# Kernel optimization log

Hardware: AMD Instinct MI355X
Metric: run time of the kernel (lower is better)

Reference implementation:

```python
import jax, jax.numpy as jnp
import numpy as np

EPS = 1e-5

def _ln(x, g, b):
    m = jnp.mean(x, axis=-1, keepdims=True)
    v = jnp.var(x, axis=-1, keepdims=True)
    return (x - m) * jax.lax.rsqrt(v + EPS) * g + b

def _lrelu(x):
    return jnp.where(x >= 0, x, 0.2 * x)

def _xavier(k, shape):
    a = (6.0 / (shape[0] + shape[1])) ** 0.5
    return jax.random.uniform(k, shape, minval=-a, maxval=a, dtype=jnp.float32)

def setup_inputs() -> dict:
    key = jax.random.key(0)
    ks = jax.random.split(key, 10)
    B, P, I = 32, 2048, 4096          # batch, n_pathway, n_img_features
    HQ, QK, HV, L = 64, 64, 64, 256   # hidden_dim_q(==qk), hidden_dim_qk, hidden_dim_v, classifier latent
    return {
        "img": jax.random.normal(ks[0], (B, 4, I), jnp.float32),
        "pathway": jax.random.normal(ks[1], (B, P), jnp.float32),
        "qw": _xavier(ks[2], (1, HQ)),
        "qw2": _xavier(ks[3], (HQ, QK)),
        "kw": _xavier(ks[4], (4, QK)),
        "vw": _xavier(ks[5], (4, HV)),
        "vw2": jax.random.normal(ks[6], (HV, 1), jnp.float32) * (HV ** -0.5),
        "q_g": jnp.ones(QK, jnp.float32), "q_b": jnp.zeros(QK, jnp.float32),
        "k_g": jnp.ones(QK, jnp.float32), "k_b": jnp.zeros(QK, jnp.float32),
        "v_g": jnp.ones(HV, jnp.float32), "v_b": jnp.zeros(HV, jnp.float32),
        "n1_g": jnp.ones(P, jnp.float32), "n1_b": jnp.zeros(P, jnp.float32),
        "n2_g": jnp.ones(L, jnp.float32), "n2_b": jnp.zeros(L, jnp.float32),
        "w1": _xavier(ks[7], (L, P)), "b1": jnp.zeros(L, jnp.float32),
        "w2": jax.random.normal(ks[8], (1, L), jnp.float32) * (L ** -0.5),
        "b2": jnp.zeros(1, jnp.float32),
    }

def reference(img, pathway, qw, qw2, kw, vw, vw2,
              q_g, q_b, k_g, k_b, v_g, v_b, n1_g, n1_b, n2_g, n2_b,
              w1, b1, w2, b2):
    P = pathway.shape[1]
    vrf = (P ** 0.5) / 2.0            # gamma * sqrt(n_pathway) / 2, gamma=1.0
    C = 0.5                           # soft_sign_constant
    img_t = jnp.swapaxes(img, -2, -1)              # [B, I, 4]
    # query path: outer product with [1, HQ] weight, LN, leaky, second proj, leaky (source applies key_relu to query)
    qm = pathway[..., None] @ qw                   # [B, P, HQ]
    qm = _lrelu(_ln(qm, q_g, q_b))
    qm = _lrelu(qm @ qw2)                          # [B, P, QK]
    # key path: LN only (source never relu's the key matrix)
    km = _ln(img_t @ kw, k_g, k_b)                 # [B, I, QK]
    # value path
    vm = _lrelu(_ln(img_t @ vw, v_g, v_b)) @ vw2   # [B, I, 1]
    # relu + variance-scale + soft-sign attention
    attn = jnp.einsum('bpd,bid->bpi', qm, km)      # [B, P, I]
    attn = jax.nn.relu(attn) / vrf
    attn = attn / (jnp.abs(attn) + C)
    out = attn @ vm                                # [B, P, 1]
    # classifier head (dropout = identity in eval)
    h = _lrelu(_ln(out[..., 0], n1_g, n1_b))       # [B, P]
    h = _lrelu(_ln(h @ w1.T + b1, n2_g, n2_b))     # [B, L]
    logits = h @ w2.T + b2                         # [B, 1]
    return (logits, attn, out)
```

## Files before the change

### kernel.cpp

```cpp
#include <hip/hip_runtime.h>
#include <hip/hip_bf16.h>

#define EPS 1e-5f
#define INV_VRF 4.4194173824159220e-02f

#define NB 32
#define NP 2048
#define NI 4096
#define ND 64
#define NL 256

#define ATTN_OFF 32L
#define OUT_OFF  268435488L

typedef __attribute__((ext_vector_type(4))) float vf4;
typedef __attribute__((ext_vector_type(4))) short vs4;
typedef __attribute__((ext_vector_type(8))) short vs8;

__device__ __forceinline__ unsigned short f2bf(float f) {
  unsigned int u = __float_as_uint(f);
  unsigned int r = (u + 0x7FFFu + ((u >> 16) & 1u)) >> 16;
  return (unsigned short)r;
}

__device__ __forceinline__ void gload16(const void* g, void* l) {
  __builtin_amdgcn_global_load_lds(
      (const __attribute__((address_space(1))) unsigned int*)g,
      (__attribute__((address_space(3))) unsigned int*)l, 16, 0, 0);
}

__global__ __launch_bounds__(256) void k_qm(
    const float* __restrict__ pathway, const float* __restrict__ qw,
    const float* __restrict__ qw2, const float* __restrict__ q_g,
    const float* __restrict__ q_b, unsigned short* __restrict__ qm)
{
  __shared__ float qw2s[64 * 64];
  int tid = threadIdx.x, lane = tid & 63, w = tid >> 6;
  for (int idx = tid; idx < 4096; idx += 256) qw2s[idx] = qw2[idx];
  float qwv = qw[lane], qg = q_g[lane], qb = q_b[lane];
  float s1 = qwv, s2 = qwv * qwv;
  #pragma unroll
  for (int m = 32; m; m >>= 1) { s1 += __shfl_xor(s1, m); s2 += __shfl_xor(s2, m); }
  float mq = s1 * (1.f / 64.f), vq = s2 * (1.f / 64.f) - mq * mq;
  float qc = qwv - mq;
  __syncthreads();
  long base = (long)blockIdx.x * 32 + w * 8;
  for (int r = 0; r < 8; ++r) {
    long row = base + r;
    float s = pathway[row];
    float alpha = s * rsqrtf(s * s * vq + EPS);
    float t = alpha * qc * qg + qb;
    t = t >= 0.f ? t : 0.2f * t;
    float acc = 0.f;
    #pragma unroll
    for (int h = 0; h < 64; ++h) acc += __shfl(t, h) * qw2s[h * 64 + lane];
    acc = acc >= 0.f ? acc : 0.2f * acc;
    qm[row * 64 + lane] = f2bf(acc);
  }
}

__global__ __launch_bounds__(256) void k_kmvm(
    const float* __restrict__ img, const float* __restrict__ kw,
    const float* __restrict__ vw, const float* __restrict__ vw2,
    const float* __restrict__ k_g, const float* __restrict__ k_b,
    const float* __restrict__ v_g, const float* __restrict__ v_b,
    unsigned short* __restrict__ km, float* __restrict__ vm)
{
  int tid = threadIdx.x, lane = tid & 63, w = tid >> 6;
  long row = (long)blockIdx.x * 4 + w;
  int b = (int)(row >> 12), i = (int)(row & 4095);
  const float* ib = img + (long)b * 4 * 4096 + i;
  float xv = (lane < 4) ? ib[lane * 4096] : 0.f;
  float x0 = __shfl(xv, 0), x1 = __shfl(xv, 1), x2 = __shfl(xv, 2), x3 = __shfl(xv, 3);
  int d = lane;
  float kp = x0 * kw[d] + x1 * kw[64 + d] + x2 * kw[128 + d] + x3 * kw[192 + d];
  float vp = x0 * vw[d] + x1 * vw[64 + d] + x2 * vw[128 + d] + x3 * vw[192 + d];
  float a1 = kp, a2 = kp * kp, a3 = vp, a4 = vp * vp;
  #pragma unroll
  for (int m = 32; m; m >>= 1) {
    a1 += __shfl_xor(a1, m); a2 += __shfl_xor(a2, m);
    a3 += __shfl_xor(a3, m); a4 += __shfl_xor(a4, m);
  }
  float mk = a1 * (1.f / 64.f), vk = a2 * (1.f / 64.f) - mk * mk;
  float mv = a3 * (1.f / 64.f), vv = a4 * (1.f / 64.f) - mv * mv;
  float kmv = (kp - mk) * rsqrtf(vk + EPS) * k_g[d] + k_b[d];
  km[row * 64 + d] = f2bf(kmv);
  float y = (vp - mv) * rsqrtf(vv + EPS) * v_g[d] + v_b[d];
  y = y >= 0.f ? y : 0.2f * y;
  float pv = y * vw2[d];
  #pragma unroll
  for (int m = 32; m; m >>= 1) pv += __shfl_xor(pv, m);
  if (lane == 0) vm[row] = pv;
}

__global__ __launch_bounds__(256) void k_attn(
    const unsigned short* __restrict__ qm, const unsigned short* __restrict__ km,
    const float* __restrict__ vm, float* __restrict__ dout)
{
  __shared__ __align__(16) unsigned short qm_s[64 * 64];
  __shared__ __align__(16) unsigned short km_s[2][64 * 64];
  int tid = threadIdx.x, lane = tid & 63, w = tid >> 6;
  int g = lane >> 4, c = lane & 15;
  int bid = blockIdx.x, b = bid >> 5, pt = bid & 31;
  long p_base = (long)b * NP + pt * 64;
  const char* qsrc = (const char*)(qm + p_base * 64);
  const char* ksrc = (const char*)(km + (long)b * NI * 64);

  #pragma unroll
  for (int j = 0; j < 2; ++j) {
    int o = w * 2048 + j * 1024 + (lane << 4);
    gload16(qsrc + o, (char*)qm_s + w * 2048 + j * 1024);
  }
  #pragma unroll
  for (int j = 0; j < 2; ++j) {
    int o = w * 2048 + j * 1024 + (lane << 4);
    int so = o ^ ((((o >> 7) & 7)) << 4);
    gload16(ksrc + so, (char*)km_s[0] + w * 2048 + j * 1024);
  }
  __syncthreads();

  vs8 afr[2];
  {
    const char* qrow = (const char*)qm_s + (w * 16 + c) * 128;
    #pragma unroll
    for (int kk = 0; kk < 2; ++kk) {
      vs4 lo = *(const vs4*)(qrow + kk * 64 + 8 * g);
      vs4 hi = *(const vs4*)(qrow + kk * 64 + 32 + 8 * g);
      vs8 a;
      a[0] = lo[0]; a[1] = lo[1]; a[2] = lo[2]; a[3] = lo[3];
      a[4] = hi[0]; a[5] = hi[1]; a[6] = hi[2]; a[7] = hi[3];
      afr[kk] = a;
    }
  }
  float* rp[4];
  #pragma unroll
  for (int r = 0; r < 4; ++r)
    rp[r] = dout + ATTN_OFF + (p_base + w * 16 + g * 4 + r) * (long)NI;
  const float* vmb = vm + (long)b * NI;
  float oacc[4] = {0.f, 0.f, 0.f, 0.f};
  int swz = (c & 7) << 4;

  for (int s = 0; s < 64; ++s) {
    int cur = s & 1;
    if (s < 63) {
      #pragma unroll
      for (int j = 0; j < 2; ++j) {
        int o = w * 2048 + j * 1024 + (lane << 4);
        int so = o ^ ((((o >> 7) & 7)) << 4);
        gload16(ksrc + (s + 1) * 8192 + so,
                (char*)km_s[cur ^ 1] + w * 2048 + j * 1024);
      }
    }
    vf4 acc[4];
    #pragma unroll
    for (int nt = 0; nt < 4; ++nt) acc[nt] = (vf4){0.f, 0.f, 0.f, 0.f};
    #pragma unroll
    for (int kk = 0; kk < 2; ++kk) {
      #pragma unroll
      for (int nt = 0; nt < 4; ++nt) {
        const char* krow = (const char*)km_s[cur] + (nt * 16 + c) * 128;
        vs4 lo = *(const vs4*)(krow + ((kk * 64 + 8 * g) ^ swz));
        vs4 hi = *(const vs4*)(krow + ((kk * 64 + 32 + 8 * g) ^ swz));
        vs8 bf;
        bf[0] = lo[0]; bf[1] = lo[1]; bf[2] = lo[2]; bf[3] = lo[3];
        bf[4] = hi[0]; bf[5] = hi[1]; bf[6] = hi[2]; bf[7] = hi[3];
        acc[nt] = __builtin_amdgcn_mfma_f32_16x16x32_bf16(afr[kk], bf, acc[nt], 0, 0, 0);
      }
    }
    int ib0 = s * 64;
    float vmv[4];
    #pragma unroll
    for (int nt = 0; nt < 4; ++nt) vmv[nt] = vmb[ib0 + nt * 16 + c];
    #pragma unroll
    for (int r = 0; r < 4; ++r) {
      float* rpr = rp[r];
      #pragma unroll
      for (int nt = 0; nt < 4; ++nt) {
        int col = ib0 + nt * 16 + c;
        float x = acc[nt][r];
        x = fmaxf(x, 0.f) * INV_VRF;
        float y = x * __builtin_amdgcn_rcpf(x + 0.5f);
        rpr[col] = y;
        oacc[r] += y * vmv[nt];
      }
    }
    __syncthreads();
  }
  #pragma unroll
  for (int m = 1; m <= 8; m <<= 1) {
    #pragma unroll
    for (int r = 0; r < 4; ++r) oacc[r] += __shfl_xor(oacc[r], m);
  }
  if (c == 0) {
    #pragma unroll
    for (int r = 0; r < 4; ++r)
      dout[OUT_OFF + p_base + w * 16 + g * 4 + r] = oacc[r];
  }
}

__global__ __launch_bounds__(256) void k_head(
    const float* __restrict__ n1_g, const float* __restrict__ n1_b,
    const float* __restrict__ n2_g, const float* __restrict__ n2_b,
    const float* __restrict__ w1, const float* __restrict__ b1,
    const float* __restrict__ w2, const float* __restrict__ b2,
    float* __restrict__ dout)
{
  int tid = threadIdx.x, lane = tid & 63, w = tid >> 6;
  int b = blockIdx.x;
  __shared__ float h1s[2048];
  __shared__ float red[8];
  const float* orow = dout + OUT_OFF + (long)b * NP;
  float vals[8];
  float s1 = 0.f, s2 = 0.f;
  #pragma unroll
  for (int j = 0; j < 8; ++j) {
    float v = orow[j * 256 + tid];
    vals[j] = v; s1 += v; s2 += v * v;
  }
  #pragma unroll
  for (int m = 32; m; m >>= 1) { s1 += __shfl_xor(s1, m); s2 += __shfl_xor(s2, m); }
  if (lane == 0) { red[w] = s1; red[4 + w] = s2; }
  __syncthreads();
  float S1 = red[0] + red[1] + red[2] + red[3];
  float S2 = red[4] + red[5] + red[6] + red[7];
  float mean = S1 * (1.f / 2048.f);
  float var = S2 * (1.f / 2048.f) - mean * mean;
  float rs = rsqrtf(var + EPS);
  __syncthreads();
  #pragma unroll
  for (int j = 0; j < 8; ++j) {
    int p = j * 256 + tid;
    float h = (vals[j] - mean) * rs * n1_g[p] + n1_b[p];
    h = h >= 0.f ? h : 0.2f * h;
    h1s[p] = h;
  }
  __syncthreads();
  float acc = b1[tid];
  const float* wr = w1 + (long)tid * 2048;
  for (int q = 0; q < 2048; q += 4) {
    float4 wv = *(const float4*)(wr + q);
    acc += wv.x * h1s[q] + wv.y * h1s[q + 1] + wv.z * h1s[q + 2] + wv.w * h1s[q + 3];
  }
  float t1 = acc, t2 = acc * acc;
  #pragma unroll
  for (int m = 32; m; m >>= 1) { t1 += __shfl_xor(t1, m); t2 += __shfl_xor(t2, m); }
  if (lane == 0) { red[w] = t1; red[4 + w] = t2; }
  __syncthreads();
  float T1 = red[0] + red[1] + red[2] + red[3];
  float T2 = red[4] + red[5] + red[6] + red[7];
  float m2 = T1 * (1.f / 256.f);
  float v2 = T2 * (1.f / 256.f) - m2 * m2;
  float rs2 = rsqrtf(v2 + EPS);
  float h2 = (acc - m2) * rs2 * n2_g[tid] + n2_b[tid];
  h2 = h2 >= 0.f ? h2 : 0.2f * h2;
  float lg = h2 * w2[tid];
  #pragma unroll
  for (int m = 32; m; m >>= 1) lg += __shfl_xor(lg, m);
  __syncthreads();
  if (lane == 0) red[w] = lg;
  __syncthreads();
  if (tid == 0) dout[b] = red[0] + red[1] + red[2] + red[3] + b2[0];
}

extern "C" void kernel_launch(void* const* d_in, const int* in_sizes, int n_in,
                              void* d_out, int out_size, void* d_ws, size_t ws_size,
                              hipStream_t stream)
{
  const float* img     = (const float*)d_in[0];
  const float* pathway = (const float*)d_in[1];
  const float* qw      = (const float*)d_in[2];
  const float* qw2     = (const float*)d_in[3];
  const float* kw      = (const float*)d_in[4];
  const float* vw      = (const float*)d_in[5];
  const float* vw2     = (const float*)d_in[6];
  const float* q_g     = (const float*)d_in[7];
  const float* q_b     = (const float*)d_in[8];
  const float* k_g     = (const float*)d_in[9];
  const float* k_b     = (const float*)d_in[10];
  const float* v_g     = (const float*)d_in[11];
  const float* v_b     = (const float*)d_in[12];
  const float* n1_g    = (const float*)d_in[13];
  const float* n1_b    = (const float*)d_in[14];
  const float* n2_g    = (const float*)d_in[15];
  const float* n2_b    = (const float*)d_in[16];
  const float* w1      = (const float*)d_in[17];
  const float* b1      = (const float*)d_in[18];
  const float* w2      = (const float*)d_in[19];
  const float* b2      = (const float*)d_in[20];
  float* dout = (float*)d_out;

  unsigned short* qm_ws = (unsigned short*)d_ws;
  unsigned short* km_ws = (unsigned short*)((char*)d_ws + 8388608);
  float*          vm_ws = (float*)((char*)d_ws + 25165824);

  k_qm<<<dim3(2048), dim3(256), 0, stream>>>(pathway, qw, qw2, q_g, q_b, qm_ws);
  k_kmvm<<<dim3(32768), dim3(256), 0, stream>>>(img, kw, vw, vw2, k_g, k_b, v_g, v_b, km_ws, vm_ws);
  k_attn<<<dim3(1024), dim3(256), 0, stream>>>(qm_ws, km_ws, vm_ws, dout);
  k_head<<<dim3(32), dim3(256), 0, stream>>>(n1_g, n1_b, n2_g, n2_b, w1, b1, w2, b2, dout);
}
```

Measured before the change: 500.3 us.

## Transpose attn tile through LDS for vectorized nontemporal stores, remap blocks

The attention kernel now stages each MFMA output tile through a per-wave swizzled LDS buffer, so every lane writes 16-byte contiguous chunks of attn with nontemporal stores instead of scattered 4-byte stores. The vm loads become float4, and the out reduction shrinks to two shuffles. The block index is remapped (bid&7)*128 + bid>>3, likely to spread batches across XCDs for better L2 locality of km. The __syncthreads are replaced by explicit waitcnt/s_barrier, and the partial vmcnt(8) wait is meant to let stores stay in flight across iterations. These manual waitcnt counts carry a correctness risk if the instruction ordering changes.

```diff
diff --git a/kernel.cpp b/kernel.cpp
--- a/kernel.cpp
+++ b/kernel.cpp
@@ -99,9 +99,12 @@
 {
   __shared__ __align__(16) unsigned short qm_s[64 * 64];
   __shared__ __align__(16) unsigned short km_s[2][64 * 64];
+  __shared__ __align__(16) float tr_s[4][1024];
   int tid = threadIdx.x, lane = tid & 63, w = tid >> 6;
   int g = lane >> 4, c = lane & 15;
-  int bid = blockIdx.x, b = bid >> 5, pt = bid & 31;
+  int bid = blockIdx.x;
+  int lbid = (bid & 7) * 128 + (bid >> 3);
+  int b = lbid >> 5, pt = lbid & 31;
   long p_base = (long)b * NP + pt * 64;
   const char* qsrc = (const char*)(qm + p_base * 64);
   const char* ksrc = (const char*)(km + (long)b * NI * 64);
@@ -110,14 +113,11 @@
   for (int j = 0; j < 2; ++j) {
     int o = w * 2048 + j * 1024 + (lane << 4);
     gload16(qsrc + o, (char*)qm_s + w * 2048 + j * 1024);
-  }
-  #pragma unroll
-  for (int j = 0; j < 2; ++j) {
-    int o = w * 2048 + j * 1024 + (lane << 4);
     int so = o ^ ((((o >> 7) & 7)) << 4);
     gload16(ksrc + so, (char*)km_s[0] + w * 2048 + j * 1024);
   }
-  __syncthreads();
+  asm volatile("s_waitcnt vmcnt(0)" ::: "memory");
+  __builtin_amdgcn_s_barrier();
 
   vs8 afr[2];
   {
@@ -132,12 +132,11 @@
       afr[kk] = a;
     }
   }
-  float* rp[4];
-  #pragma unroll
-  for (int r = 0; r < 4; ++r)
-    rp[r] = dout + ATTN_OFF + (p_base + w * 16 + g * 4 + r) * (long)NI;
-  const float* vmb = vm + (long)b * NI;
-  float oacc[4] = {0.f, 0.f, 0.f, 0.f};
+  int q = lane & 3, row = lane >> 2;
+  float* rowp = dout + ATTN_OFF + (p_base + w * 16 + row) * (long)NI + q * 4;
+  const float* vmq = vm + (long)b * NI + q * 4;
+  float* trw = tr_s[w];
+  float oacc = 0.f;
   int swz = (c & 7) << 4;
 
   for (int s = 0; s < 64; ++s) {
@@ -151,6 +150,8 @@
                 (char*)km_s[cur ^ 1] + w * 2048 + j * 1024);
       }
     }
+    __builtin_amdgcn_sched_barrier(0);
+
     vf4 acc[4];
     #pragma unroll
     for (int nt = 0; nt < 4; ++nt) acc[nt] = (vf4){0.f, 0.f, 0.f, 0.f};
@@ -167,35 +168,33 @@
         acc[nt] = __builtin_amdgcn_mfma_f32_16x16x32_bf16(afr[kk], bf, acc[nt], 0, 0, 0);
       }
     }
-    int ib0 = s * 64;
-    float vmv[4];
-    #pragma unroll
-    for (int nt = 0; nt < 4; ++nt) vmv[nt] = vmb[ib0 + nt * 16 + c];
-    #pragma unroll
-    for (int r = 0; r < 4; ++r) {
-      float* rpr = rp[r];
+    #pragma unroll
+    for (int nt = 0; nt < 4; ++nt) {
       #pragma unroll
-      for (int nt = 0; nt < 4; ++nt) {
-        int col = ib0 + nt * 16 + c;
-        float x = acc[nt][r];
-        x = fmaxf(x, 0.f) * INV_VRF;
+      for (int r = 0; r < 4; ++r) {
+        float x = fmaxf(acc[nt][r], 0.f) * INV_VRF;
         float y = x * __builtin_amdgcn_rcpf(x + 0.5f);
-        rpr[col] = y;
-        oacc[r] += y * vmv[nt];
+        int rw = g * 4 + r;
+        int f4 = (nt * 4 + (c >> 2)) ^ rw;
+        trw[rw * 64 + f4 * 4 + (c & 3)] = y;
       }
     }
-    __syncthreads();
-  }
-  #pragma unroll
-  for (int m = 1; m <= 8; m <<= 1) {
-    #pragma unroll
-    for (int r = 0; r < 4; ++r) oacc[r] += __shfl_xor(oacc[r], m);
-  }
-  if (c == 0) {
-    #pragma unroll
-    for (int r = 0; r < 4; ++r)
-      dout[OUT_OFF + p_base + w * 16 + g * 4 + r] = oacc[r];
-  }
+    #pragma unroll
+    for (int j = 0; j < 4; ++j) {
+      int f4r = (j * 4 + q) ^ row;
+      vf4 yv = *(const vf4*)&trw[row * 64 + f4r * 4];
+      vf4 vv = *(const vf4*)(vmq + s * 64 + j * 16);
+      __builtin_nontemporal_store(yv, (vf4*)(rowp + s * 64 + j * 16));
+      oacc += yv[0] * vv[0] + yv[1] * vv[1] + yv[2] * vv[2] + yv[3] * vv[3];
+    }
+    asm volatile("s_waitcnt vmcnt(8)" ::: "memory");
+    __builtin_amdgcn_sched_barrier(0);
+    __builtin_amdgcn_s_barrier();
+  }
+  oacc += __shfl_xor(oacc, 1);
+  oacc += __shfl_xor(oacc, 2);
+  if (q == 0)
+    dout[OUT_OFF + p_base + w * 16 + row] = oacc;
 }
 
 __global__ __launch_bounds__(256) void k_head(
@@ -237,9 +236,9 @@
   __syncthreads();
   float acc = b1[tid];
   const float* wr = w1 + (long)tid * 2048;
-  for (int q = 0; q < 2048; q += 4) {
-    float4 wv = *(const float4*)(wr + q);
-    acc += wv.x * h1s[q] + wv.y * h1s[q + 1] + wv.z * h1s[q + 2] + wv.w * h1s[q + 3];
+  for (int qq = 0; qq < 2048; qq += 4) {
+    float4 wv = *(const float4*)(wr + qq);
+    acc += wv.x * h1s[qq] + wv.y * h1s[qq + 1] + wv.z * h1s[qq + 2] + wv.w * h1s[qq + 3];
   }
   float t1 = acc, t2 = acc * acc;
   #pragma unroll
```

After: 509.8 us. About the same (+1.9%).
